# Performance work log

Hardware: AMD Instinct MI355X
Metric: run time of the kernel (lower is better)

## Reference

```python
import jax, jax.numpy as jnp
import numpy as np

N_NODES = 100000
N_EDGES = 3200000
NFEAT, NHID, OPFEAT = 128, 128, 64
EPS = 1e-06


def setup_inputs() -> dict:
    key = jax.random.key(0)
    ks = jax.random.split(key, 20)
    def u(k, shape, s):
        return jax.random.uniform(k, shape, jnp.float32, -s, s)
    inp = {
        'x': jax.random.normal(ks[0], (N_NODES, NFEAT), jnp.float32),
        'edge_rows': jax.random.randint(ks[1], (N_EDGES,), 0, N_NODES, jnp.int32),
        'edge_cols': jax.random.randint(ks[2], (N_EDGES,), 0, N_NODES, jnp.int32),
        'edge_vals': jax.random.uniform(ks[3], (N_EDGES,), jnp.float32),
        # fc layers (torch Linear: weight [out, in])
        'fc1_w': u(ks[4], (NHID, NFEAT), 1.0 / np.sqrt(NFEAT)),
        'fc1_b': u(ks[5], (NHID,), 1.0 / np.sqrt(NFEAT)),
        'fc2_w': u(ks[6], (NHID, NHID), 1.0 / np.sqrt(NHID)),
        'fc2_b': u(ks[7], (NHID,), 1.0 / np.sqrt(NHID)),
        'ln_gamma': jnp.ones((NHID,), jnp.float32),
        'ln_beta': jnp.zeros((NHID,), jnp.float32),
    }
    s = 1.0 / np.sqrt(NHID)
    for i, out_f in zip(range(1, 5), [NHID, NHID, NHID, OPFEAT]):
        k1, k2, k3 = jax.random.split(jax.random.fold_in(key, 100 + i), 3)
        inp[f'gc{i}_wn'] = u(k1, (NHID, out_f), s)
        inp[f'gc{i}_ws'] = u(k2, (NHID, out_f), s)
        inp[f'gc{i}_b'] = u(k3, (out_f,), s)
    return inp


def _gcn_first_order(x, wn, ws, b, rows, cols, vals):
    # act_self + sparse_adj @ (x @ wn) + bias
    act_self = x @ ws                      # [N, out]
    support = x @ wn                       # [N, out]
    gathered = support[cols] * vals[:, None]   # [E, out] irregular gather
    act_neighbor = jax.ops.segment_sum(gathered, rows, num_segments=x.shape[0])
    return act_self + act_neighbor + b


def _layer_norm(x, gamma, beta):
    mean = jnp.mean(x, axis=-1, keepdims=True)
    std = jnp.std(x, axis=-1, keepdims=True, ddof=1)  # torch .std is unbiased
    return gamma * (x - mean) / (std + EPS) + beta


def reference(x, edge_rows, edge_cols, edge_vals,
              fc1_w, fc1_b, fc2_w, fc2_b, ln_gamma, ln_beta,
              gc1_wn, gc1_ws, gc1_b, gc2_wn, gc2_ws, gc2_b,
              gc3_wn, gc3_ws, gc3_b, gc4_wn, gc4_ws, gc4_b):
    h = jax.nn.relu(x @ fc1_w.T + fc1_b)
    h = jax.nn.relu(h @ fc2_w.T + fc2_b)
    h = _layer_norm(h, ln_gamma, ln_beta)
    h = jax.nn.relu(_gcn_first_order(h, gc1_wn, gc1_ws, gc1_b, edge_rows, edge_cols, edge_vals))
    h = jax.nn.relu(_gcn_first_order(h, gc2_wn, gc2_ws, gc2_b, edge_rows, edge_cols, edge_vals))
    h = jax.nn.relu(_gcn_first_order(h, gc3_wn, gc3_ws, gc3_b, edge_rows, edge_cols, edge_vals))
    h = jax.nn.relu(_gcn_first_order(h, gc4_wn, gc4_ws, gc4_b, edge_rows, edge_cols, edge_vals))
    return h
```

## Files before the change

### kernel.cpp

```cpp
#include <hip/hip_runtime.h>

constexpr int N_NODES = 100000;
constexpr int N_EDGES = 3200000;
constexpr float EPS = 1e-6f;

constexpr int NBKT = 196;
constexpr int BKT_SHIFT = 9;
constexpr int BKT_ROWS = 512;
constexpr int ARENA_STRIDE = 18432;
constexpr int EPB1 = 8000;
constexpr int NBLK1 = 400;
constexpr int CAP = 72;

typedef __attribute__((ext_vector_type(8))) short bfrag;
typedef __attribute__((ext_vector_type(4))) float ffrag;

__device__ __forceinline__ unsigned short f2bf(float f) {
    unsigned int u = __float_as_uint(f);
    u += 0x7FFFu + ((u >> 16) & 1u);
    return (unsigned short)(u >> 16);
}
__device__ __forceinline__ float bf_lo(unsigned int w) { return __uint_as_float(w << 16); }
__device__ __forceinline__ float bf_hi(unsigned int w) { return __uint_as_float(w & 0xFFFF0000u); }

#define FMA8(v_, s_)                                                          \
    acc[0] = fmaf(v_, bf_lo(s_.x), acc[0]); acc[1] = fmaf(v_, bf_hi(s_.x), acc[1]); \
    acc[2] = fmaf(v_, bf_lo(s_.y), acc[2]); acc[3] = fmaf(v_, bf_hi(s_.y), acc[3]); \
    acc[4] = fmaf(v_, bf_lo(s_.z), acc[4]); acc[5] = fmaf(v_, bf_hi(s_.z), acc[5]); \
    acc[6] = fmaf(v_, bf_lo(s_.w), acc[6]); acc[7] = fmaf(v_, bf_hi(s_.w), acc[7]);

__global__ __launch_bounds__(256) void prep_w_k(
    const float* __restrict__ fc1_w, const float* __restrict__ fc2_w,
    const float* __restrict__ wn0, const float* __restrict__ ws0,
    const float* __restrict__ wn1, const float* __restrict__ ws1,
    const float* __restrict__ wn2, const float* __restrict__ ws2,
    const float* __restrict__ wn3, const float* __restrict__ ws3,
    unsigned short* __restrict__ Wb)
{
    int idx = blockIdx.x * 256 + threadIdx.x;
    if (idx >= 147456) return;
    float v;
    if (idx < 32768) {
        int r = idx >> 7, k = idx & 127;
        v = (r < 128) ? fc1_w[r * 128 + k] : fc2_w[(r - 128) * 128 + k];
    } else if (idx < 131072) {
        int idx2 = idx - 32768;
        int l = idx2 >> 15, w = idx2 & 32767;
        int o = w >> 8, k = w & 255;
        const float* wn = l == 0 ? wn0 : l == 1 ? wn1 : wn2;
        const float* ws = l == 0 ? ws0 : l == 1 ? ws1 : ws2;
        v = (k < 128) ? ws[k * 128 + o] : wn[(k - 128) * 128 + o];
    } else {
        int idx3 = idx - 131072;
        int o = idx3 >> 7, k = idx3 & 127;
        v = (o < 64) ? wn3[k * 64 + o] : ws3[k * 64 + (o - 64)];
    }
    Wb[idx] = f2bf(v);
}

__global__ __launch_bounds__(256) void front_k(
    const int* __restrict__ rows, const int* __restrict__ cols,
    const float* __restrict__ vals, int* gcur,
    unsigned* __restrict__ arena_e, unsigned short* __restrict__ arena_r,
    const float* __restrict__ x, const float* __restrict__ fc1_w,
    const float* __restrict__ fc1_b, unsigned short* __restrict__ Yb)
{
    __shared__ __align__(16) char smem[59136];
    const int tid = threadIdx.x;

    if (blockIdx.x < NBLK1) {
        int* hist   = (int*)smem;
        int* lstart = hist + NBKT;
        int* lcur   = lstart + NBKT;
        int* gbase  = lcur + NBKT;
        unsigned* st_e        = (unsigned*)(gbase + NBKT);
        unsigned short* st_r  = (unsigned short*)(st_e + EPB1);
        unsigned char* st_b   = (unsigned char*)(st_r + EPB1);
        const int e0 = blockIdx.x * EPB1;
        const int ecnt = min(EPB1, N_EDGES - e0);

        for (int i = tid; i < NBKT; i += 256) hist[i] = 0;
        __syncthreads();
        for (int i = tid; i < ecnt; i += 256)
            atomicAdd(&hist[rows[e0 + i] >> BKT_SHIFT], 1);
        __syncthreads();
        if (tid == 0) {
            int s = 0;
            for (int b = 0; b < NBKT; b++) { lstart[b] = s; s += hist[b]; }
        }
        __syncthreads();
        for (int i = tid; i < NBKT; i += 256) lcur[i] = lstart[i];
        __syncthreads();
        for (int i = tid; i < ecnt; i += 256) {
            int r = rows[e0 + i];
            int b = r >> BKT_SHIFT;
            unsigned entry = ((unsigned)cols[e0 + i] << 15)
                           | (unsigned)(f2bf(vals[e0 + i]) & 0x7FFF);
            int pos = atomicAdd(&lcur[b], 1);
            st_e[pos] = entry;
            st_r[pos] = (unsigned short)(r & (BKT_ROWS - 1));
            st_b[pos] = (unsigned char)b;
        }
        __syncthreads();
        for (int b = tid; b < NBKT; b += 256) {
            int cnt = lcur[b] - lstart[b];
            gbase[b] = cnt > 0 ? atomicAdd(&gcur[b], cnt) : 0;
        }
        __syncthreads();
        for (int i = tid; i < ecnt; i += 256) {
            int b = st_b[i];
            int off = gbase[b] + (i - lstart[b]);
            if (off < ARENA_STRIDE) {
                long dest = (long)b * ARENA_STRIDE + off;
                arena_e[dest] = st_e[i];
                arena_r[dest] = st_r[i];
            }
        }
        return;
    }

    unsigned short* Bs = (unsigned short*)smem;
    for (int i = tid; i < 16384; i += 256) {
        int n = i >> 7, k = i & 127;
        Bs[n * 136 + k] = f2bf(fc1_w[i]);
    }
    const int wave = tid >> 6, lane = tid & 63;
    const int quad = lane >> 4, l16 = lane & 15;
    const long base = (long)(blockIdx.x - NBLK1) * 128 + wave * 32;

    union AU { uint4 q; bfrag v; unsigned short s[8]; };
    bfrag a[2][4];
#pragma unroll
    for (int mt = 0; mt < 2; mt++) {
        long node = base + mt * 16 + l16;
        bool ok = node < N_NODES;
        const float4* Ar = (const float4*)(x + node * 128);
#pragma unroll
        for (int t = 0; t < 4; t++) {
            AU u;
            if (ok) {
                float4 f0 = Ar[t * 8 + quad * 2];
                float4 f1 = Ar[t * 8 + quad * 2 + 1];
                u.s[0] = f2bf(f0.x); u.s[1] = f2bf(f0.y);
                u.s[2] = f2bf(f0.z); u.s[3] = f2bf(f0.w);
                u.s[4] = f2bf(f1.x); u.s[5] = f2bf(f1.y);
                u.s[6] = f2bf(f1.z); u.s[7] = f2bf(f1.w);
            } else u.q = make_uint4(0, 0, 0, 0);
            a[mt][t] = u.v;
        }
    }
    __syncthreads();

    ffrag acc[2][8];
#pragma unroll
    for (int mt = 0; mt < 2; mt++)
#pragma unroll
        for (int nt = 0; nt < 8; nt++) acc[mt][nt] = (ffrag)0.f;

#pragma unroll
    for (int t = 0; t < 4; t++)
#pragma unroll
        for (int nt = 0; nt < 8; nt++) {
            bfrag b = *(const bfrag*)&Bs[(nt * 16 + l16) * 136 + t * 32 + quad * 8];
            acc[0][nt] = __builtin_amdgcn_mfma_f32_16x16x32_bf16(a[0][t], b, acc[0][nt], 0, 0, 0);
            acc[1][nt] = __builtin_amdgcn_mfma_f32_16x16x32_bf16(a[1][t], b, acc[1][nt], 0, 0, 0);
        }

    float bv[8];
#pragma unroll
    for (int nt = 0; nt < 8; nt++) bv[nt] = fc1_b[nt * 16 + l16];
#pragma unroll
    for (int mt = 0; mt < 2; mt++)
#pragma unroll
        for (int reg = 0; reg < 4; reg++) {
            long node = base + mt * 16 + quad * 4 + reg;
            if (node >= N_NODES) continue;
#pragma unroll
            for (int nt = 0; nt < 8; nt++)
                Yb[node * 128 + nt * 16 + l16] = f2bf(fmaxf(acc[mt][nt][reg] + bv[nt], 0.f));
        }
}

template<int MODE>
__global__ __launch_bounds__(256, 2) void mfma_gemm_k(
    const void* Av, const unsigned short* __restrict__ Wg_,
    const float* __restrict__ bias,
    const float* __restrict__ gamma, const float* __restrict__ beta,
    unsigned short* __restrict__ Yb, float* Tout)
{
    constexpr int NT = 8;
    __shared__ unsigned short Bs[128 * 136];
    const int tid = threadIdx.x;

    const uint4* Wg = (const uint4*)Wg_;
    uint4* Bs4 = (uint4*)Bs;
    for (int i = tid; i < 128 * 16; i += 256) {
        int n = i >> 4, c = i & 15;
        Bs4[n * 17 + c] = Wg[i];
    }

    const int wave = tid >> 6, lane = tid & 63;
    const int quad = lane >> 4, l16 = lane & 15;
    const long base = (long)blockIdx.x * 128 + wave * 32;

    union AU { uint4 q; bfrag v; };
    bfrag a[2][4];
#pragma unroll
    for (int mt = 0; mt < 2; mt++) {
        long node = base + mt * 16 + l16;
        bool ok = node < N_NODES;
        const uint4* Ar = (const uint4*)((const unsigned short*)Av + node * 128);
#pragma unroll
        for (int t = 0; t < 4; t++) {
            AU u;
            u.q = ok ? Ar[t * 4 + quad] : make_uint4(0, 0, 0, 0);
            a[mt][t] = u.v;
        }
    }
    __syncthreads();

    ffrag acc[2][NT];
#pragma unroll
    for (int mt = 0; mt < 2; mt++)
#pragma unroll
        for (int nt = 0; nt < NT; nt++) acc[mt][nt] = (ffrag)0.f;

#pragma unroll
    for (int t = 0; t < 4; t++)
#pragma unroll
        for (int nt = 0; nt < NT; nt++) {
            bfrag b = *(const bfrag*)&Bs[(nt * 16 + l16) * 136 + t * 32 + quad * 8];
            acc[0][nt] = __builtin_amdgcn_mfma_f32_16x16x32_bf16(a[0][t], b, acc[0][nt], 0, 0, 0);
            acc[1][nt] = __builtin_amdgcn_mfma_f32_16x16x32_bf16(a[1][t], b, acc[1][nt], 0, 0, 0);
        }

    if (MODE == 1) {
        float bv[NT], gv[NT], bev[NT];
#pragma unroll
        for (int nt = 0; nt < NT; nt++) {
            bv[nt] = bias[nt * 16 + l16];
            gv[nt] = gamma[nt * 16 + l16];
            bev[nt] = beta[nt * 16 + l16];
        }
#pragma unroll
        for (int mt = 0; mt < 2; mt++)
#pragma unroll
            for (int reg = 0; reg < 4; reg++) {
                long node = base + mt * 16 + quad * 4 + reg;
                if (node >= N_NODES) continue;
                float v[NT], s = 0.f, sq = 0.f;
#pragma unroll
                for (int nt = 0; nt < NT; nt++) {
                    v[nt] = fmaxf(acc[mt][nt][reg] + bv[nt], 0.f);
                    s += v[nt]; sq += v[nt] * v[nt];
                }
#pragma unroll
                for (int off = 1; off < 16; off <<= 1) {
                    s  += __shfl_xor(s, off, 64);
                    sq += __shfl_xor(sq, off, 64);
                }
                float mean = s * (1.f / 128.f);
                float var = fmaxf((sq - 128.f * mean * mean) * (1.f / 127.f), 0.f);
                float inv = 1.f / (sqrtf(var) + EPS);
#pragma unroll
                for (int nt = 0; nt < NT; nt++)
                    Yb[node * 128 + nt * 16 + l16] = f2bf(gv[nt] * (v[nt] - mean) * inv + bev[nt]);
            }
    } else {
        float bv[4];
#pragma unroll
        for (int i = 0; i < 4; i++) bv[i] = bias[i * 16 + l16];
#pragma unroll
        for (int mt = 0; mt < 2; mt++)
#pragma unroll
            for (int reg = 0; reg < 4; reg++) {
                long node = base + mt * 16 + quad * 4 + reg;
                if (node >= N_NODES) continue;
#pragma unroll
                for (int nt = 0; nt < 4; nt++)
                    Yb[node * 64 + nt * 16 + l16] = f2bf(acc[mt][nt][reg]);
#pragma unroll
                for (int nt = 4; nt < 8; nt++)
                    Tout[node * 64 + (nt - 4) * 16 + l16] = acc[mt][nt][reg] + bv[nt - 4];
            }
    }
}

__global__ __launch_bounds__(512, 1) void fused_gemm_k(
    const unsigned short* __restrict__ A1, const unsigned short* __restrict__ A2,
    const unsigned short* __restrict__ Wg_, const float* __restrict__ bias,
    unsigned short* __restrict__ Y)
{
    constexpr int NT = 8;
    __shared__ unsigned short Bs[128 * 264];
    const int tid = threadIdx.x;

    const uint4* Wg = (const uint4*)Wg_;
    uint4* Bs4 = (uint4*)Bs;
    for (int i = tid; i < 128 * 32; i += 512) {
        int n = i >> 5, c = i & 31;
        Bs4[n * 33 + c] = Wg[i];
    }

    const int wave = tid >> 6, lane = tid & 63;
    const int quad = lane >> 4, l16 = lane & 15;
    const long base = (long)blockIdx.x * 256 + wave * 32;

    union AU { uint4 q; bfrag v; };
    bfrag a[2][8];
#pragma unroll
    for (int mt = 0; mt < 2; mt++) {
        long node = base + mt * 16 + l16;
        bool ok = node < N_NODES;
        const uint4* A1r = (const uint4*)(A1 + node * 128);
        const uint4* A2r = (const uint4*)(A2 + node * 128);
#pragma unroll
        for (int t = 0; t < 4; t++) {
            AU u1, u2;
            u1.q = ok ? A1r[t * 4 + quad] : make_uint4(0, 0, 0, 0);
            u2.q = ok ? A2r[t * 4 + quad] : make_uint4(0, 0, 0, 0);
            a[mt][t] = u1.v;
            a[mt][4 + t] = u2.v;
        }
    }
    __syncthreads();

    ffrag acc[2][NT];
#pragma unroll
    for (int mt = 0; mt < 2; mt++)
#pragma unroll
        for (int nt = 0; nt < NT; nt++) acc[mt][nt] = (ffrag)0.f;

#pragma unroll
    for (int t = 0; t < 8; t++)
#pragma unroll
        for (int nt = 0; nt < NT; nt++) {
            bfrag b = *(const bfrag*)&Bs[(nt * 16 + l16) * 264 + t * 32 + quad * 8];
            acc[0][nt] = __builtin_amdgcn_mfma_f32_16x16x32_bf16(a[0][t], b, acc[0][nt], 0, 0, 0);
            acc[1][nt] = __builtin_amdgcn_mfma_f32_16x16x32_bf16(a[1][t], b, acc[1][nt], 0, 0, 0);
        }

    float bv[NT];
#pragma unroll
    for (int nt = 0; nt < NT; nt++) bv[nt] = bias[nt * 16 + l16];
#pragma unroll
    for (int mt = 0; mt < 2; mt++)
#pragma unroll
        for (int reg = 0; reg < 4; reg++) {
            long node = base + mt * 16 + quad * 4 + reg;
            if (node >= N_NODES) continue;
#pragma unroll
            for (int nt = 0; nt < NT; nt++)
                Y[node * 128 + nt * 16 + l16] = f2bf(fmaxf(acc[mt][nt][reg] + bv[nt], 0.f));
        }
}

__global__ __launch_bounds__(1024) void build_k(
    const int* __restrict__ gcur, const unsigned* __restrict__ arena_e,
    const unsigned short* __restrict__ arena_r,
    unsigned* __restrict__ csr, int* __restrict__ cursor)
{
    __shared__ int cnt[BKT_ROWS];
    const int tid = threadIdx.x;
    const int b = blockIdx.x;
    for (int i = tid; i < BKT_ROWS; i += 1024) cnt[i] = 0;
    __syncthreads();
    const int ec = min(gcur[b], ARENA_STRIDE);
    const long abase = (long)b * ARENA_STRIDE;
    for (int i = tid; i < ec; i += 1024) {
        unsigned entry = arena_e[abase + i];
        int rib = arena_r[abase + i] & (BKT_ROWS - 1);
        int rank = atomicAdd(&cnt[rib], 1);
        if (rank < CAP)
            csr[((long)b * BKT_ROWS + rib) * CAP + rank] = entry;
    }
    __syncthreads();
    for (int i = tid; i < BKT_ROWS; i += 1024) {
        int gr = b * BKT_ROWS + i;
        if (gr < N_NODES) cursor[gr] = min(cnt[i], CAP);
    }
}

__global__ __launch_bounds__(256) void gather_k(
    const int* __restrict__ cursor, const unsigned* __restrict__ csr,
    const unsigned short* __restrict__ Sb, unsigned short* __restrict__ G)
{
    int node = blockIdx.x * 4 + (threadIdx.x >> 6);
    if (node >= N_NODES) return;
    int lane = threadIdx.x & 63;
    int fl = lane & 15, ep = lane >> 4;
    const long s = (long)node * CAP;
    const int total = min(cursor[node], CAP);

    float acc[8] = {0, 0, 0, 0, 0, 0, 0, 0};
    const uint4* S4 = (const uint4*)Sb;

    for (int base = 0; base < total; base += 64) {
        int idx = base + lane;
        unsigned ed = (idx < total) ? csr[s + idx] : 0u;
        int cnt = total - base; if (cnt > 64) cnt = 64;
        int U = cnt >> 4;
        int j = ep;
        for (int u = 0; u < U; u++, j += 16) {
            unsigned p0 = (unsigned)__shfl((int)ed, j, 64);
            unsigned p1 = (unsigned)__shfl((int)ed, j + 4, 64);
            unsigned p2 = (unsigned)__shfl((int)ed, j + 8, 64);
            unsigned p3 = (unsigned)__shfl((int)ed, j + 12, 64);
            float v0 = __uint_as_float((p0 & 0x7FFFu) << 16);
            float v1 = __uint_as_float((p1 & 0x7FFFu) << 16);
            float v2 = __uint_as_float((p2 & 0x7FFFu) << 16);
            float v3 = __uint_as_float((p3 & 0x7FFFu) << 16);
            uint4 s0 = S4[((p0 >> 15) << 4) + fl];
            uint4 s1 = S4[((p1 >> 15) << 4) + fl];
            uint4 s2 = S4[((p2 >> 15) << 4) + fl];
            uint4 s3 = S4[((p3 >> 15) << 4) + fl];
            { float v = v0; uint4 q = s0; float* accp = acc; (void)accp;
              acc[0] = fmaf(v, bf_lo(q.x), acc[0]); acc[1] = fmaf(v, bf_hi(q.x), acc[1]);
              acc[2] = fmaf(v, bf_lo(q.y), acc[2]); acc[3] = fmaf(v, bf_hi(q.y), acc[3]);
              acc[4] = fmaf(v, bf_lo(q.z), acc[4]); acc[5] = fmaf(v, bf_hi(q.z), acc[5]);
              acc[6] = fmaf(v, bf_lo(q.w), acc[6]); acc[7] = fmaf(v, bf_hi(q.w), acc[7]); }
            { float v = v1; uint4 q = s1;
              acc[0] = fmaf(v, bf_lo(q.x), acc[0]); acc[1] = fmaf(v, bf_hi(q.x), acc[1]);
              acc[2] = fmaf(v, bf_lo(q.y), acc[2]); acc[3] = fmaf(v, bf_hi(q.y), acc[3]);
              acc[4] = fmaf(v, bf_lo(q.z), acc[4]); acc[5] = fmaf(v, bf_hi(q.z), acc[5]);
              acc[6] = fmaf(v, bf_lo(q.w), acc[6]); acc[7] = fmaf(v, bf_hi(q.w), acc[7]); }
            { float v = v2; uint4 q = s2;
              acc[0] = fmaf(v, bf_lo(q.x), acc[0]); acc[1] = fmaf(v, bf_hi(q.x), acc[1]);
              acc[2] = fmaf(v, bf_lo(q.y), acc[2]); acc[3] = fmaf(v, bf_hi(q.y), acc[3]);
              acc[4] = fmaf(v, bf_lo(q.z), acc[4]); acc[5] = fmaf(v, bf_hi(q.z), acc[5]);
              acc[6] = fmaf(v, bf_lo(q.w), acc[6]); acc[7] = fmaf(v, bf_hi(q.w), acc[7]); }
            { float v = v3; uint4 q = s3;
              acc[0] = fmaf(v, bf_lo(q.x), acc[0]); acc[1] = fmaf(v, bf_hi(q.x), acc[1]);
              acc[2] = fmaf(v, bf_lo(q.y), acc[2]); acc[3] = fmaf(v, bf_hi(q.y), acc[3]);
              acc[4] = fmaf(v, bf_lo(q.z), acc[4]); acc[5] = fmaf(v, bf_hi(q.z), acc[5]);
              acc[6] = fmaf(v, bf_lo(q.w), acc[6]); acc[7] = fmaf(v, bf_hi(q.w), acc[7]); }
        }
        int T = (cnt - (U << 4) + 3) >> 2;
        for (int t = 0; t < T; t++, j += 4) {
            unsigned p0 = (unsigned)__shfl((int)ed, j, 64);
            float v0 = __uint_as_float((p0 & 0x7FFFu) << 16);
            uint4 s0 = S4[((p0 >> 15) << 4) + fl];
            FMA8(v0, s0)
        }
    }
#pragma unroll
    for (int off = 16; off < 64; off <<= 1)
#pragma unroll
        for (int j = 0; j < 8; j++) acc[j] += __shfl_xor(acc[j], off, 64);

    if (ep == 0) {
        uint4 p;
        p.x = (unsigned)f2bf(acc[0]) | ((unsigned)f2bf(acc[1]) << 16);
        p.y = (unsigned)f2bf(acc[2]) | ((unsigned)f2bf(acc[3]) << 16);
        p.z = (unsigned)f2bf(acc[4]) | ((unsigned)f2bf(acc[5]) << 16);
        p.w = (unsigned)f2bf(acc[6]) | ((unsigned)f2bf(acc[7]) << 16);
        ((uint4*)G)[node * 16 + fl] = p;
    }
}

__global__ __launch_bounds__(256) void gather64_k(
    const int* __restrict__ cursor, const unsigned* __restrict__ csr,
    const unsigned short* __restrict__ Sb, const float* __restrict__ T,
    float* __restrict__ out)
{
    int node = blockIdx.x * 4 + (threadIdx.x >> 6);
    if (node >= N_NODES) return;
    int lane = threadIdx.x & 63;
    int fl = lane & 7, ep = lane >> 3;
    const long s = (long)node * CAP;
    const int total = min(cursor[node], CAP);

    float acc[8] = {0, 0, 0, 0, 0, 0, 0, 0};
    const uint4* S4 = (const uint4*)Sb;

    for (int base = 0; base < total; base += 64) {
        int idx = base + lane;
        unsigned ed = (idx < total) ? csr[s + idx] : 0u;
        int cnt = total - base; if (cnt > 64) cnt = 64;
        int U = cnt >> 4;
        int j = ep;
        for (int u = 0; u < U; u++, j += 16) {
            unsigned p0 = (unsigned)__shfl((int)ed, j, 64);
            unsigned p1 = (unsigned)__shfl((int)ed, j + 8, 64);
            float v0 = __uint_as_float((p0 & 0x7FFFu) << 16);
            float v1 = __uint_as_float((p1 & 0x7FFFu) << 16);
            uint4 s0 = S4[((p0 >> 15) << 3) + fl];
            uint4 s1 = S4[((p1 >> 15) << 3) + fl];
            FMA8(v0, s0) FMA8(v1, s1)
        }
        int TT = (cnt - (U << 4) + 7) >> 3;
        for (int t = 0; t < TT; t++, j += 8) {
            unsigned p0 = (unsigned)__shfl((int)ed, j, 64);
            float v0 = __uint_as_float((p0 & 0x7FFFu) << 16);
            uint4 s0 = S4[((p0 >> 15) << 3) + fl];
            FMA8(v0, s0)
        }
    }
#pragma unroll
    for (int off = 8; off < 64; off <<= 1)
#pragma unroll
        for (int j = 0; j < 8; j++) acc[j] += __shfl_xor(acc[j], off, 64);

    if (ep == 0) {
        const float4* T4 = (const float4*)T;
        float4 t0 = T4[(long)node * 16 + fl * 2];
        float4 t1 = T4[(long)node * 16 + fl * 2 + 1];
        float4 o0, o1;
        o0.x = fmaxf(acc[0] + t0.x, 0.f); o0.y = fmaxf(acc[1] + t0.y, 0.f);
        o0.z = fmaxf(acc[2] + t0.z, 0.f); o0.w = fmaxf(acc[3] + t0.w, 0.f);
        o1.x = fmaxf(acc[4] + t1.x, 0.f); o1.y = fmaxf(acc[5] + t1.y, 0.f);
        o1.z = fmaxf(acc[6] + t1.z, 0.f); o1.w = fmaxf(acc[7] + t1.w, 0.f);
        ((float4*)out)[(long)node * 16 + fl * 2]     = o0;
        ((float4*)out)[(long)node * 16 + fl * 2 + 1] = o1;
    }
}

extern "C" void kernel_launch(void* const* d_in, const int* in_sizes, int n_in,
                              void* d_out, int out_size, void* d_ws, size_t ws_size,
                              hipStream_t stream)
{
    const float* x     = (const float*)d_in[0];
    const int*   erows = (const int*)d_in[1];
    const int*   ecols = (const int*)d_in[2];
    const float* evals = (const float*)d_in[3];
    const float* fc1_w = (const float*)d_in[4];
    const float* fc1_b = (const float*)d_in[5];
    const float* fc2_w = (const float*)d_in[6];
    const float* fc2_b = (const float*)d_in[7];
    const float* ln_g  = (const float*)d_in[8];
    const float* ln_b  = (const float*)d_in[9];
    const float* gc_wn[4] = {(const float*)d_in[10], (const float*)d_in[13],
                             (const float*)d_in[16], (const float*)d_in[19]};
    const float* gc_ws[4] = {(const float*)d_in[11], (const float*)d_in[14],
                             (const float*)d_in[17], (const float*)d_in[20]};
    const float* gc_b[4]  = {(const float*)d_in[12], (const float*)d_in[15],
                             (const float*)d_in[18], (const float*)d_in[21]};

    unsigned short* Abf = (unsigned short*)d_ws;
    unsigned short* Gbf = Abf + (size_t)N_NODES * 128;
    unsigned* csr = (unsigned*)(Gbf + (size_t)N_NODES * 128);
    unsigned* arena_e = csr + (size_t)N_NODES * CAP;
    unsigned short* arena_r =
        (unsigned short*)(arena_e + (size_t)NBKT * ARENA_STRIDE);
    unsigned short* Wb = arena_r + (size_t)NBKT * ARENA_STRIDE;
    int* cursor = (int*)(Wb + 147456);
    int* gcur   = cursor + N_NODES;
    float* Tf   = (float*)Abf;
    float* out = (float*)d_out;

    dim3 blk(256);
    int gemm_grid = (N_NODES + 127) / 128;
    int fg_grid   = (N_NODES + 255) / 256;
    int node_grid = (N_NODES + 3) / 4;

    hipMemsetAsync(gcur, 0, NBKT * 4, stream);
    front_k<<<NBLK1 + gemm_grid, blk, 0, stream>>>(
        erows, ecols, evals, gcur, arena_e, arena_r,
        x, fc1_w, fc1_b, Gbf);

    prep_w_k<<<(147456 + 255) / 256, blk, 0, stream>>>(
        fc1_w, fc2_w, gc_wn[0], gc_ws[0], gc_wn[1], gc_ws[1],
        gc_wn[2], gc_ws[2], gc_wn[3], gc_ws[3], Wb);

    build_k<<<NBKT, dim3(1024), 0, stream>>>(gcur, arena_e, arena_r, csr, cursor);

    mfma_gemm_k<1><<<gemm_grid, blk, 0, stream>>>(
        Gbf, Wb + 16384, fc2_b, ln_g, ln_b, Abf, nullptr);

    for (int l = 0; l < 3; l++) {
        gather_k<<<node_grid, blk, 0, stream>>>(cursor, csr, Abf, Gbf);
        fused_gemm_k<<<fg_grid, dim3(512), 0, stream>>>(
            Abf, Gbf, Wb + 32768 + l * 32768, gc_b[l], Abf);
    }

    mfma_gemm_k<2><<<gemm_grid, blk, 0, stream>>>(
        Abf, Wb + 131072, gc_b[3], nullptr, nullptr, Gbf, Tf);
    gather64_k<<<node_grid, blk, 0, stream>>>(cursor, csr, Gbf, Tf, out);
}
```

Before: 685.1 us.

## Sort CSR entries within each row by column bin for gather locality

The CSR build now does a two-pass counting sort inside each row, binning entries by the top bits of the packed column index (e>>27), so each row's neighbours are laid out in roughly ascending column order. The goal is better cache locality in the gather kernel, since nearby wavefronts then touch similar regions of the support matrix. The cost is a second pass over the arena, a larger shared histogram (512x26 ints) and a per-row prefix scan. The gather's FMA blocks are also collapsed into the macro, which is cosmetic.

```diff
diff --git a/kernel.cpp b/kernel.cpp
--- a/kernel.cpp
+++ b/kernel.cpp
@@ -11,6 +11,7 @@
 constexpr int EPB1 = 8000;
 constexpr int NBLK1 = 400;
 constexpr int CAP = 72;
+constexpr int NBIN = 25;
 
 typedef __attribute__((ext_vector_type(8))) short bfrag;
 typedef __attribute__((ext_vector_type(4))) float ffrag;
@@ -360,24 +361,42 @@
     const unsigned short* __restrict__ arena_r,
     unsigned* __restrict__ csr, int* __restrict__ cursor)
 {
-    __shared__ int cnt[BKT_ROWS];
+    __shared__ int cnt[BKT_ROWS][NBIN + 1];
     const int tid = threadIdx.x;
     const int b = blockIdx.x;
-    for (int i = tid; i < BKT_ROWS; i += 1024) cnt[i] = 0;
+    for (int i = tid; i < BKT_ROWS * (NBIN + 1); i += 1024)
+        ((int*)cnt)[i] = 0;
     __syncthreads();
     const int ec = min(gcur[b], ARENA_STRIDE);
     const long abase = (long)b * ARENA_STRIDE;
+
     for (int i = tid; i < ec; i += 1024) {
-        unsigned entry = arena_e[abase + i];
         int rib = arena_r[abase + i] & (BKT_ROWS - 1);
-        int rank = atomicAdd(&cnt[rib], 1);
-        if (rank < CAP)
-            csr[((long)b * BKT_ROWS + rib) * CAP + rank] = entry;
-    }
-    __syncthreads();
-    for (int i = tid; i < BKT_ROWS; i += 1024) {
-        int gr = b * BKT_ROWS + i;
-        if (gr < N_NODES) cursor[gr] = min(cnt[i], CAP);
+        int bin = arena_e[abase + i] >> 27;
+        atomicAdd(&cnt[rib][bin], 1);
+    }
+    __syncthreads();
+    for (int r = tid; r < BKT_ROWS; r += 1024) {
+        int s = 0;
+#pragma unroll
+        for (int bi = 0; bi < NBIN; bi++) {
+            int c = cnt[r][bi]; cnt[r][bi] = s; s += c;
+        }
+        cnt[r][NBIN] = s;
+    }
+    __syncthreads();
+    for (int i = tid; i < ec; i += 1024) {
+        unsigned e = arena_e[abase + i];
+        int rib = arena_r[abase + i] & (BKT_ROWS - 1);
+        int bin = e >> 27;
+        int pos = atomicAdd(&cnt[rib][bin], 1);
+        if (pos < CAP)
+            csr[((long)b * BKT_ROWS + rib) * CAP + pos] = e;
+    }
+    __syncthreads();
+    for (int r = tid; r < BKT_ROWS; r += 1024) {
+        int gr = b * BKT_ROWS + r;
+        if (gr < N_NODES) cursor[gr] = min(cnt[r][NBIN], CAP);
     }
 }
 
@@ -414,26 +433,7 @@
             uint4 s1 = S4[((p1 >> 15) << 4) + fl];
             uint4 s2 = S4[((p2 >> 15) << 4) + fl];
             uint4 s3 = S4[((p3 >> 15) << 4) + fl];
-            { float v = v0; uint4 q = s0; float* accp = acc; (void)accp;
-              acc[0] = fmaf(v, bf_lo(q.x), acc[0]); acc[1] = fmaf(v, bf_hi(q.x), acc[1]);
-              acc[2] = fmaf(v, bf_lo(q.y), acc[2]); acc[3] = fmaf(v, bf_hi(q.y), acc[3]);
-              acc[4] = fmaf(v, bf_lo(q.z), acc[4]); acc[5] = fmaf(v, bf_hi(q.z), acc[5]);
-              acc[6] = fmaf(v, bf_lo(q.w), acc[6]); acc[7] = fmaf(v, bf_hi(q.w), acc[7]); }
-            { float v = v1; uint4 q = s1;
-              acc[0] = fmaf(v, bf_lo(q.x), acc[0]); acc[1] = fmaf(v, bf_hi(q.x), acc[1]);
-              acc[2] = fmaf(v, bf_lo(q.y), acc[2]); acc[3] = fmaf(v, bf_hi(q.y), acc[3]);
-              acc[4] = fmaf(v, bf_lo(q.z), acc[4]); acc[5] = fmaf(v, bf_hi(q.z), acc[5]);
-              acc[6] = fmaf(v, bf_lo(q.w), acc[6]); acc[7] = fmaf(v, bf_hi(q.w), acc[7]); }
-            { float v = v2; uint4 q = s2;
-              acc[0] = fmaf(v, bf_lo(q.x), acc[0]); acc[1] = fmaf(v, bf_hi(q.x), acc[1]);
-              acc[2] = fmaf(v, bf_lo(q.y), acc[2]); acc[3] = fmaf(v, bf_hi(q.y), acc[3]);
-              acc[4] = fmaf(v, bf_lo(q.z), acc[4]); acc[5] = fmaf(v, bf_hi(q.z), acc[5]);
-              acc[6] = fmaf(v, bf_lo(q.w), acc[6]); acc[7] = fmaf(v, bf_hi(q.w), acc[7]); }
-            { float v = v3; uint4 q = s3;
-              acc[0] = fmaf(v, bf_lo(q.x), acc[0]); acc[1] = fmaf(v, bf_hi(q.x), acc[1]);
-              acc[2] = fmaf(v, bf_lo(q.y), acc[2]); acc[3] = fmaf(v, bf_hi(q.y), acc[3]);
-              acc[4] = fmaf(v, bf_lo(q.z), acc[4]); acc[5] = fmaf(v, bf_hi(q.z), acc[5]);
-              acc[6] = fmaf(v, bf_lo(q.w), acc[6]); acc[7] = fmaf(v, bf_hi(q.w), acc[7]); }
+            FMA8(v0, s0) FMA8(v1, s1) FMA8(v2, s2) FMA8(v3, s3)
         }
         int T = (cnt - (U << 4) + 3) >> 2;
         for (int t = 0; t < T; t++, j += 4) {
```

Result: no change. 695.1 us (+1.5%).
